# Kernel optimization log

Hardware: AMD Instinct MI355X
Metric: run time of the kernel (lower is better)

The kernel has to match this reference:

```python
import jax, jax.numpy as jnp
import numpy as np

NEG_INF = -9.0e15
ALPHA = 0.2  # leakyrelu slope


def setup_inputs() -> dict:
    key = jax.random.key(0)
    k1, k2, k3, k4, k5 = jax.random.split(key, 5)
    B, N, D_IN, D_OUT = 8, 2048, 128, 128
    h = jax.random.normal(k1, (B, N, D_IN), dtype=jnp.float32)
    adj = jax.random.randint(k2, (N, N), 0, 2, dtype=jnp.int32)
    W = jax.random.normal(k3, (D_IN, D_OUT), dtype=jnp.float32) * (1.0 / np.sqrt(D_IN))
    a_src = jax.random.normal(k4, (D_OUT,), dtype=jnp.float32) * (1.0 / np.sqrt(D_OUT))
    a_dst = jax.random.normal(k5, (D_OUT,), dtype=jnp.float32) * (1.0 / np.sqrt(D_OUT))
    return {"h": h, "adj": adj, "W": W, "a_src": a_src, "a_dst": a_dst}


def reference(h, adj, W, a_src, a_dst):
    # Wh: [B, N, D_out]
    Wh = jnp.einsum("bnd,de->bne", h, W)
    e_src = jnp.einsum("bne,e->bn", Wh, a_src)  # [B, N]
    e_dst = jnp.einsum("bne,e->bn", Wh, a_dst)  # [B, N]
    # additive attention logits: e[b,i,j] = e_src[b,i] + e_dst[b,j]
    e = e_src[:, :, None] + e_dst[:, None, :]  # [B, N, N]
    e = jnp.where(e > 0, e, ALPHA * e)  # leaky relu
    e = jnp.where(adj[None, :, :] > 0, e, NEG_INF)
    attention = jax.nn.softmax(e, axis=-1)  # [B, N, N]
    h_prime = jnp.einsum("bij,bje->bie", attention, Wh)
    return h_prime
```

## Files before the change

### kernel.cpp

```cpp
#include <hip/hip_runtime.h>
#include <stdint.h>

#define ALPHA 0.2f
#define LOG2E 1.4426950408889634f

typedef unsigned short u16;
typedef short s16x8 __attribute__((ext_vector_type(8)));
typedef float f32x4 __attribute__((ext_vector_type(4)));

union BF8 { s16x8 v; uint32_t u[4]; u16 s[8]; uint4 q; };

static __device__ __forceinline__ float bf2f(u16 u) {
  union { uint32_t i; float f; } c; c.i = ((uint32_t)u) << 16; return c.f;
}
static __device__ __forceinline__ uint32_t pk2bf(float lo, float hi) {
  uint32_t ul = __float_as_uint(lo) + 0x8000u;
  uint32_t uh = __float_as_uint(hi) + 0x8000u;
  return (ul >> 16) | (uh & 0xffff0000u);
}

static __device__ __forceinline__ void gl2lds16(const void* g, void* l) {
  __builtin_amdgcn_global_load_lds(
      (const __attribute__((address_space(1))) uint32_t*)g,
      (__attribute__((address_space(3))) uint32_t*)l, 16, 0, 0);
}

__global__ __launch_bounds__(256) void k_zero(uint32_t* __restrict__ out, int n32) {
  int gid = blockIdx.x * 256 + threadIdx.x;
  if (gid < n32) out[gid] = 0u;
}

__global__ __launch_bounds__(256) void k_prep(
    const int* __restrict__ adj, uint32_t* __restrict__ bits,
    const void* __restrict__ hV, const void* __restrict__ WgV,
    const void* __restrict__ aSrcV, const void* __restrict__ aDstV,
    int* __restrict__ flag,
    u16* __restrict__ WhT, float* __restrict__ eS, float* __restrict__ eD) {
  __shared__ __align__(16) char smemRaw[34816];
  __shared__ float aS[128], aD[128];

  const int tid = threadIdx.x;
  const int bk = blockIdx.x;

  if (bk >= 256) {
    const int pk = bk - 256;
    int base = pk * 256 + tid;
#pragma unroll
    for (int it = 0; it < 8; ++it) {
      int gid = base + it * (2048 * 256);
      unsigned long long m = __ballot(adj[gid] != 0);
      if ((tid & 63) == 0)
        *(unsigned long long*)(&bits[gid >> 5]) = m;
    }
    if (pk == 0 && tid < 64) {
      u16 v = ((const u16*)hV)[2 * tid];
      int e = (v >> 7) & 0xff;
      unsigned long long dm = __ballot(e >= 100 && e <= 140);
      if (tid == 0) flag[0] = (__popcll(dm) >= 48) ? 1 : 0;
    }
    return;
  }

  u16*   WT   = (u16*)smemRaw;
  float* tile = (float*)smemRaw;
  const int mb = bk * 64;

  int isBf;
  {
    u16 v = ((const u16*)hV)[2 * (tid & 63)];
    int e = (v >> 7) & 0xff;
    unsigned long long dm = __ballot(e >= 100 && e <= 140);
    isBf = (__popcll(dm) >= 48) ? 1 : 0;
  }

  if (isBf) {
    const u16* Wg = (const u16*)WgV;
    for (int it = 0; it < 8; ++it) {
      int idx = tid + it * 256;
      int k = idx >> 4, c0 = (idx & 15) * 8;
      uint4 w4 = *(const uint4*)(Wg + (k << 7) + c0);
      u16* wsv = (u16*)&w4;
#pragma unroll
      for (int e = 0; e < 8; ++e) WT[(c0 + e) * 136 + k] = wsv[e];
    }
    if (tid < 128) aS[tid] = bf2f(((const u16*)aSrcV)[tid]);
    else           aD[tid - 128] = bf2f(((const u16*)aDstV)[tid - 128]);
  } else {
    const float* Wg = (const float*)WgV;
    for (int it = 0; it < 8; ++it) {
      int idx = tid + it * 256;
      int k = idx >> 4, c0 = (idx & 15) * 8;
      float4 w0 = *(const float4*)(Wg + (k << 7) + c0);
      float4 w1 = *(const float4*)(Wg + (k << 7) + c0 + 4);
      float wf[8] = {w0.x, w0.y, w0.z, w0.w, w1.x, w1.y, w1.z, w1.w};
#pragma unroll
      for (int e = 0; e < 8; ++e)
        WT[(c0 + e) * 136 + k] = (u16)((__float_as_uint(wf[e]) + 0x8000u) >> 16);
    }
    if (tid < 128) aS[tid] = ((const float*)aSrcV)[tid];
    else           aD[tid - 128] = ((const float*)aDstV)[tid - 128];
  }
  __syncthreads();

  const int wv = tid >> 6, lane = tid & 63, ln = lane & 15, quad = lane >> 4;
  const int row = mb + wv * 16 + ln;

  f32x4 acc[8];
#pragma unroll
  for (int t = 0; t < 8; ++t) acc[t] = (f32x4){0.f, 0.f, 0.f, 0.f};

  if (isBf) {
    const u16* h = (const u16*)hV;
#pragma unroll
    for (int ks = 0; ks < 4; ++ks) {
      s16x8 af = *(const s16x8*)(h + (row << 7) + ks * 32 + quad * 8);
#pragma unroll
      for (int t = 0; t < 8; ++t) {
        s16x8 bfg = *(const s16x8*)(&WT[(t * 16 + ln) * 136 + ks * 32 + quad * 8]);
        acc[t] = __builtin_amdgcn_mfma_f32_16x16x32_bf16(af, bfg, acc[t], 0, 0, 0);
      }
    }
  } else {
    const float* h = (const float*)hV;
#pragma unroll
    for (int ks = 0; ks < 4; ++ks) {
      float4 a0 = *(const float4*)(h + (row << 7) + ks * 32 + quad * 8);
      float4 a1 = *(const float4*)(h + (row << 7) + ks * 32 + quad * 8 + 4);
      BF8 af;
      af.u[0] = pk2bf(a0.x, a0.y);
      af.u[1] = pk2bf(a0.z, a0.w);
      af.u[2] = pk2bf(a1.x, a1.y);
      af.u[3] = pk2bf(a1.z, a1.w);
#pragma unroll
      for (int t = 0; t < 8; ++t) {
        s16x8 bfg = *(const s16x8*)(&WT[(t * 16 + ln) * 136 + ks * 32 + quad * 8]);
        acc[t] = __builtin_amdgcn_mfma_f32_16x16x32_bf16(af.v, bfg, acc[t], 0, 0, 0);
      }
    }
  }
  __syncthreads();

#pragma unroll
  for (int t = 0; t < 8; ++t)
#pragma unroll
    for (int r = 0; r < 4; ++r)
      tile[(wv * 16 + quad * 4 + r) * 130 + t * 16 + ln] = acc[t][r];
  __syncthreads();

  if (tid < 128) {
    int r = tid & 63, grp = tid >> 6;
    const float* a = grp ? aD : aS;
    float sum = 0.f;
#pragma unroll 4
    for (int d = 0; d < 128; ++d) sum += tile[r * 130 + d] * a[d];
    int m = mb + r, b = m >> 11, n = m & 2047;
    (grp ? eD : eS)[(b << 11) + n] = sum * LOG2E;
  }

  {
    int d = tid >> 1, half = tid & 1;
    int n0 = mb & 2047, b = mb >> 11;
    uint32_t pk[16];
#pragma unroll
    for (int qq = 0; qq < 16; ++qq) {
      float v0 = tile[(half * 32 + 2 * qq) * 130 + d];
      float v1 = tile[(half * 32 + 2 * qq + 1) * 130 + d];
      pk[qq] = pk2bf(v0, v1);
    }
    uint4* dst = (uint4*)(WhT + (size_t)((b << 7) + d) * 2048 + n0 + half * 32);
#pragma unroll
    for (int c = 0; c < 4; ++c)
      dst[c] = make_uint4(pk[c * 4], pk[c * 4 + 1], pk[c * 4 + 2], pk[c * 4 + 3]);
  }
}

__global__ __launch_bounds__(512, 4) void k_attn(
    const u16* __restrict__ WhT, const float* __restrict__ eSrc,
    const float* __restrict__ eDst, const uint32_t* __restrict__ adjBits,
    const int* __restrict__ flag, void* __restrict__ outV) {
  __shared__ __align__(16) u16 bufB[2][8192];
  __shared__ __align__(16) u16 bufP[2][2048];

  const int tid = threadIdx.x;
  const int bid = (blockIdx.x & 7) * 64 + (blockIdx.x >> 3);
  const int b = bid >> 6, ig = bid & 63;
  const int i0 = ig * 32;

  const int w = tid >> 6, l = tid & 63;
  const int ln = l & 15, quad = l >> 4;
  const int s = w & 1, dh = w >> 1;

  const int gsrc = (l & 7) ^ ((l >> 3) & 7);
  const u16* whtB = WhT + ((size_t)b << 18);
  const u16* srcB = whtB + (size_t)(w * 8 + (l >> 3)) * 2048 + gsrc * 8;

  const int prow = tid >> 4, hg = tid & 15;
  const float sSp = eSrc[(b << 11) + i0 + prow];
  const float* eDb = eDst + (b << 11) + hg * 4;
  const uint32_t* adjB = adjBits + (size_t)(i0 + prow) * 64 + (hg >> 3);
  const int pOff = prow * 128 + ((hg ^ ((prow & 7) << 1)) * 8);

  const int aOff0 = (s * 16 + ln) * 128 + (((0 * 4 + quad) ^ (ln & 7)) * 16);
  const int aOff1 = (s * 16 + ln) * 128 + (((1 * 4 + quad) ^ (ln & 7)) * 16);
  const int bOff00 = (dh * 32 + 0 * 16 + ln) * 128 + (((0 * 4 + quad) ^ (ln & 7)) * 16);
  const int bOff10 = (dh * 32 + 1 * 16 + ln) * 128 + (((0 * 4 + quad) ^ (ln & 7)) * 16);
  const int bOff01 = (dh * 32 + 0 * 16 + ln) * 128 + (((1 * 4 + quad) ^ (ln & 7)) * 16);
  const int bOff11 = (dh * 32 + 1 * 16 + ln) * 128 + (((1 * 4 + quad) ^ (ln & 7)) * 16);

  f32x4 acc0 = (f32x4){0.f, 0.f, 0.f, 0.f};
  f32x4 acc1 = (f32x4){0.f, 0.f, 0.f, 0.f};
  f32x4 accD = (f32x4){0.f, 0.f, 0.f, 0.f};

  BF8 ones;
  ones.u[0] = 0x3f803f80u; ones.u[1] = 0x3f803f80u;
  ones.u[2] = 0x3f803f80u; ones.u[3] = 0x3f803f80u;

#define PPROD(dv, aw, pdst)  {                                                \
    uint32_t nib = ((aw) >> ((hg & 7) * 4)) & 0xfu;                           \
    float x0 = sSp + (dv)[0], x1 = sSp + (dv)[1];                             \
    float x2 = sSp + (dv)[2], x3 = sSp + (dv)[3];                             \
    float p0 = exp2f(__builtin_amdgcn_fmed3f(x0, ALPHA * x0, 80.f));          \
    float p1 = exp2f(__builtin_amdgcn_fmed3f(x1, ALPHA * x1, 80.f));          \
    float p2 = exp2f(__builtin_amdgcn_fmed3f(x2, ALPHA * x2, 80.f));          \
    float p3 = exp2f(__builtin_amdgcn_fmed3f(x3, ALPHA * x3, 80.f));          \
    uint32_t m01 = ((nib & 1u) ? 0x0000ffffu : 0u) | ((nib & 2u) ? 0xffff0000u : 0u); \
    uint32_t m23 = ((nib & 4u) ? 0x0000ffffu : 0u) | ((nib & 8u) ? 0xffff0000u : 0u); \
    *(uint2*)((char*)(pdst) + pOff) = make_uint2(pk2bf(p0, p1) & m01,         \
                                                 pk2bf(p2, p3) & m23);        \
  }

#define CONSUME(pPc, pBc)  {                                                  \
    s16x8 af0 = *(const s16x8*)((const char*)(pPc) + aOff0);                  \
    s16x8 af1 = *(const s16x8*)((const char*)(pPc) + aOff1);                  \
    s16x8 b00 = *(const s16x8*)((const char*)(pBc) + bOff00);                 \
    s16x8 b10 = *(const s16x8*)((const char*)(pBc) + bOff10);                 \
    s16x8 b01 = *(const s16x8*)((const char*)(pBc) + bOff01);                 \
    s16x8 b11 = *(const s16x8*)((const char*)(pBc) + bOff11);                 \
    __builtin_amdgcn_s_setprio(1);                                            \
    acc0 = __builtin_amdgcn_mfma_f32_16x16x32_bf16(af0, b00, acc0, 0, 0, 0);  \
    acc1 = __builtin_amdgcn_mfma_f32_16x16x32_bf16(af0, b10, acc1, 0, 0, 0);  \
    acc0 = __builtin_amdgcn_mfma_f32_16x16x32_bf16(af1, b01, acc0, 0, 0, 0);  \
    acc1 = __builtin_amdgcn_mfma_f32_16x16x32_bf16(af1, b11, acc1, 0, 0, 0);  \
    if (dh == 0) {                                                            \
      accD = __builtin_amdgcn_mfma_f32_16x16x32_bf16(af0, ones.v, accD, 0, 0, 0); \
      accD = __builtin_amdgcn_mfma_f32_16x16x32_bf16(af1, ones.v, accD, 0, 0, 0); \
    }                                                                         \
    __builtin_amdgcn_s_setprio(0);                                            \
  }

  u16 *bBc = bufB[0], *bBn = bufB[1];
  u16 *bPc = bufP[0], *bPn = bufP[1];

  gl2lds16(srcB, bBc + w * 512);
  gl2lds16(srcB + 131072, bBc + 4096 + w * 512);
  {
    f32x4 dv = *(const f32x4*)(eDb);
    uint32_t aw = adjB[0];
    PPROD(dv, aw, bPc);
  }
  __syncthreads();

  for (int t = 0; t < 32; ++t) {
    if (t + 1 < 32) {
      gl2lds16(srcB + (size_t)(t + 1) * 64, bBn + w * 512);
      gl2lds16(srcB + (size_t)(t + 1) * 64 + 131072, bBn + 4096 + w * 512);
      f32x4 dv = *(const f32x4*)(eDb + (t + 1) * 64);
      uint32_t aw = adjB[(t + 1) * 2];
      PPROD(dv, aw, bPn);
    }
    CONSUME(bPc, bBc);
    __syncthreads();
    u16* tb = bBc; bBc = bBn; bBn = tb;
    u16* tp = bPc; bPc = bPn; bPn = tp;
  }

  float* den = (float*)bufP;
  if (dh == 0 && ln == 0) {
#pragma unroll
    for (int r = 0; r < 4; ++r) den[s * 16 + quad * 4 + r] = accD[r];
  }
  __syncthreads();

  float inv[4];
#pragma unroll
  for (int r = 0; r < 4; ++r)
    inv[r] = 1.0f / fmaxf(den[s * 16 + quad * 4 + r], 1e-37f);

  const int isBf = *flag;
  if (isBf) {
    u16* outp = (u16*)outV;
#pragma unroll
    for (int tt = 0; tt < 2; ++tt) {
      f32x4 a = tt ? acc1 : acc0;
#pragma unroll
      for (int r = 0; r < 4; ++r) {
        size_t off = ((size_t)((b << 11) + i0 + s * 16 + quad * 4 + r) << 7)
                   + dh * 32 + tt * 16 + ln;
        float v = a[r] * inv[r];
        outp[off] = (u16)((__float_as_uint(v) + 0x8000u) >> 16);
      }
    }
  } else {
    float* outp = (float*)outV;
#pragma unroll
    for (int tt = 0; tt < 2; ++tt) {
      f32x4 a = tt ? acc1 : acc0;
#pragma unroll
      for (int r = 0; r < 4; ++r) {
        size_t off = ((size_t)((b << 11) + i0 + s * 16 + quad * 4 + r) << 7)
                   + dh * 32 + tt * 16 + ln;
        outp[off] = a[r] * inv[r];
      }
    }
  }
#undef PPROD
#undef CONSUME
}

extern "C" void kernel_launch(void* const* d_in, const int* in_sizes, int n_in,
                              void* d_out, int out_size, void* d_ws, size_t ws_size,
                              hipStream_t stream) {
  const void* h   = d_in[0];
  const int* adj  = (const int*)d_in[1];
  const void* Wg  = d_in[2];
  const void* aS  = d_in[3];
  const void* aD  = d_in[4];

  const size_t OFF_ES   = (size_t)4 << 20;
  const size_t OFF_ED   = OFF_ES + (64 << 10);
  const size_t OFF_BITS = OFF_ED + (64 << 10);
  const size_t OFF_FLAG = OFF_BITS + (512 << 10);
  const size_t NEEDED   = OFF_FLAG + 64;

  if (ws_size < NEEDED) {
    int n32 = out_size / 2;
    k_zero<<<(n32 + 255) / 256, 256, 0, stream>>>((uint32_t*)d_out, n32);
    return;
  }

  char* ws = (char*)d_ws;
  u16* WhT      = (u16*)ws;
  float* eSp    = (float*)(ws + OFF_ES);
  float* eDp    = (float*)(ws + OFF_ED);
  uint32_t* bit = (uint32_t*)(ws + OFF_BITS);
  int* flag     = (int*)(ws + OFF_FLAG);

  k_prep<<<2304, 256, 0, stream>>>(adj, bit, h, Wg, aS, aD, flag, WhT, eSp, eDp);
  k_attn<<<512, 512, 0, stream>>>(WhT, eSp, eDp, bit, flag, d_out);
}
```

Baseline: 116.2 us.

## Use 32x32x16 MFMA with split-K waves and compute softmax denominator on VALU

Replaces the 16x16x32 MFMA tiling (waves split by row half and column quarter, plus extra MFMAs against a ones vector for the denominator) with 32x32x16 MFMAs, where each wave covers all 32 rows for a 32-column slice and half of the K chunk. The two K-halves are reduced through shared memory at the end. The softmax denominator is now accumulated in scalar registers from the bf16-rounded probabilities and reduced with shuffles, which removes the extra denominator MFMAs. This cuts LDS fragment loads and MFMA count per step, in exchange for a final cross-wave merge and some added VALU work in the probability stage.

```diff
diff --git a/kernel.cpp b/kernel.cpp
--- a/kernel.cpp
+++ b/kernel.cpp
@@ -7,6 +7,7 @@
 typedef unsigned short u16;
 typedef short s16x8 __attribute__((ext_vector_type(8)));
 typedef float f32x4 __attribute__((ext_vector_type(4)));
+typedef float f32x16 __attribute__((ext_vector_type(16)));
 
 union BF8 { s16x8 v; uint32_t u[4]; u16 s[8]; uint4 q; };
 
@@ -180,6 +181,7 @@
     const int* __restrict__ flag, void* __restrict__ outV) {
   __shared__ __align__(16) u16 bufB[2][8192];
   __shared__ __align__(16) u16 bufP[2][2048];
+  __shared__ float den[32];
 
   const int tid = threadIdx.x;
   const int bid = (blockIdx.x & 7) * 64 + (blockIdx.x >> 3);
@@ -187,8 +189,9 @@
   const int i0 = ig * 32;
 
   const int w = tid >> 6, l = tid & 63;
-  const int ln = l & 15, quad = l >> 4;
-  const int s = w & 1, dh = w >> 1;
+  const int dh = w & 3, jh = w >> 2;
+  const int lh = l >> 5;
+  const int xk = l & 7;
 
   const int gsrc = (l & 7) ^ ((l >> 3) & 7);
   const u16* whtB = WhT + ((size_t)b << 18);
@@ -199,23 +202,18 @@
   const float* eDb = eDst + (b << 11) + hg * 4;
   const uint32_t* adjB = adjBits + (size_t)(i0 + prow) * 64 + (hg >> 3);
   const int pOff = prow * 128 + ((hg ^ ((prow & 7) << 1)) * 8);
-
-  const int aOff0 = (s * 16 + ln) * 128 + (((0 * 4 + quad) ^ (ln & 7)) * 16);
-  const int aOff1 = (s * 16 + ln) * 128 + (((1 * 4 + quad) ^ (ln & 7)) * 16);
-  const int bOff00 = (dh * 32 + 0 * 16 + ln) * 128 + (((0 * 4 + quad) ^ (ln & 7)) * 16);
-  const int bOff10 = (dh * 32 + 1 * 16 + ln) * 128 + (((0 * 4 + quad) ^ (ln & 7)) * 16);
-  const int bOff01 = (dh * 32 + 0 * 16 + ln) * 128 + (((1 * 4 + quad) ^ (ln & 7)) * 16);
-  const int bOff11 = (dh * 32 + 1 * 16 + ln) * 128 + (((1 * 4 + quad) ^ (ln & 7)) * 16);
-
-  f32x4 acc0 = (f32x4){0.f, 0.f, 0.f, 0.f};
-  f32x4 acc1 = (f32x4){0.f, 0.f, 0.f, 0.f};
-  f32x4 accD = (f32x4){0.f, 0.f, 0.f, 0.f};
-
-  BF8 ones;
-  ones.u[0] = 0x3f803f80u; ones.u[1] = 0x3f803f80u;
-  ones.u[2] = 0x3f803f80u; ones.u[3] = 0x3f803f80u;
-
-#define PPROD(dv, aw, pdst)  {                                                \
+  float dsum = 0.f;
+
+  const int aOff0 = (l & 31) * 128 + (((jh * 4 + 0 + lh) ^ xk) * 16);
+  const int aOff1 = (l & 31) * 128 + (((jh * 4 + 2 + lh) ^ xk) * 16);
+  const int bOff0 = (dh * 32 + (l & 31)) * 128 + (((jh * 4 + 0 + lh) ^ xk) * 16);
+  const int bOff1 = (dh * 32 + (l & 31)) * 128 + (((jh * 4 + 2 + lh) ^ xk) * 16);
+
+  f32x16 acc;
+#pragma unroll
+  for (int r = 0; r < 16; ++r) acc[r] = 0.f;
+
+#define PPROD(dv, aw, pdst) {                                                 \
     uint32_t nib = ((aw) >> ((hg & 7) * 4)) & 0xfu;                           \
     float x0 = sSp + (dv)[0], x1 = sSp + (dv)[1];                             \
     float x2 = sSp + (dv)[2], x3 = sSp + (dv)[3];                             \
@@ -223,29 +221,14 @@
     float p1 = exp2f(__builtin_amdgcn_fmed3f(x1, ALPHA * x1, 80.f));          \
     float p2 = exp2f(__builtin_amdgcn_fmed3f(x2, ALPHA * x2, 80.f));          \
     float p3 = exp2f(__builtin_amdgcn_fmed3f(x3, ALPHA * x3, 80.f));          \
-    uint32_t m01 = ((nib & 1u) ? 0x0000ffffu : 0u) | ((nib & 2u) ? 0xffff0000u : 0u); \
-    uint32_t m23 = ((nib & 4u) ? 0x0000ffffu : 0u) | ((nib & 8u) ? 0xffff0000u : 0u); \
-    *(uint2*)((char*)(pdst) + pOff) = make_uint2(pk2bf(p0, p1) & m01,         \
-                                                 pk2bf(p2, p3) & m23);        \
-  }
-
-#define CONSUME(pPc, pBc)  {                                                  \
-    s16x8 af0 = *(const s16x8*)((const char*)(pPc) + aOff0);                  \
-    s16x8 af1 = *(const s16x8*)((const char*)(pPc) + aOff1);                  \
-    s16x8 b00 = *(const s16x8*)((const char*)(pBc) + bOff00);                 \
-    s16x8 b10 = *(const s16x8*)((const char*)(pBc) + bOff10);                 \
-    s16x8 b01 = *(const s16x8*)((const char*)(pBc) + bOff01);                 \
-    s16x8 b11 = *(const s16x8*)((const char*)(pBc) + bOff11);                 \
-    __builtin_amdgcn_s_setprio(1);                                            \
-    acc0 = __builtin_amdgcn_mfma_f32_16x16x32_bf16(af0, b00, acc0, 0, 0, 0);  \
-    acc1 = __builtin_amdgcn_mfma_f32_16x16x32_bf16(af0, b10, acc1, 0, 0, 0);  \
-    acc0 = __builtin_amdgcn_mfma_f32_16x16x32_bf16(af1, b01, acc0, 0, 0, 0);  \
-    acc1 = __builtin_amdgcn_mfma_f32_16x16x32_bf16(af1, b11, acc1, 0, 0, 0);  \
-    if (dh == 0) {                                                            \
-      accD = __builtin_amdgcn_mfma_f32_16x16x32_bf16(af0, ones.v, accD, 0, 0, 0); \
-      accD = __builtin_amdgcn_mfma_f32_16x16x32_bf16(af1, ones.v, accD, 0, 0, 0); \
-    }                                                                         \
-    __builtin_amdgcn_s_setprio(0);                                            \
+    p0 = (nib & 1u) ? p0 : 0.f;                                               \
+    p1 = (nib & 2u) ? p1 : 0.f;                                               \
+    p2 = (nib & 4u) ? p2 : 0.f;                                               \
+    p3 = (nib & 8u) ? p3 : 0.f;                                               \
+    uint32_t w0 = pk2bf(p0, p1), w1 = pk2bf(p2, p3);                          \
+    dsum += __uint_as_float(w0 << 16) + __uint_as_float(w0 & 0xffff0000u)     \
+          + __uint_as_float(w1 << 16) + __uint_as_float(w1 & 0xffff0000u);    \
+    *(uint2*)((char*)(pdst) + pOff) = make_uint2(w0, w1);                     \
   }
 
   u16 *bBc = bufB[0], *bBn = bufB[1];
@@ -268,53 +251,59 @@
       uint32_t aw = adjB[(t + 1) * 2];
       PPROD(dv, aw, bPn);
     }
-    CONSUME(bPc, bBc);
+    {
+      s16x8 a0 = *(const s16x8*)((const char*)bPc + aOff0);
+      s16x8 a1 = *(const s16x8*)((const char*)bPc + aOff1);
+      s16x8 f0 = *(const s16x8*)((const char*)bBc + bOff0);
+      s16x8 f1 = *(const s16x8*)((const char*)bBc + bOff1);
+      __builtin_amdgcn_s_setprio(1);
+      acc = __builtin_amdgcn_mfma_f32_32x32x16_bf16(a0, f0, acc, 0, 0, 0);
+      acc = __builtin_amdgcn_mfma_f32_32x32x16_bf16(a1, f1, acc, 0, 0, 0);
+      __builtin_amdgcn_s_setprio(0);
+    }
     __syncthreads();
     u16* tb = bBc; bBc = bBn; bBn = tb;
     u16* tp = bPc; bPc = bPn; bPn = tp;
   }
 
-  float* den = (float*)bufP;
-  if (dh == 0 && ln == 0) {
-#pragma unroll
-    for (int r = 0; r < 4; ++r) den[s * 16 + quad * 4 + r] = accD[r];
-  }
-  __syncthreads();
-
-  float inv[4];
-#pragma unroll
-  for (int r = 0; r < 4; ++r)
-    inv[r] = 1.0f / fmaxf(den[s * 16 + quad * 4 + r], 1e-37f);
-
-  const int isBf = *flag;
-  if (isBf) {
-    u16* outp = (u16*)outV;
-#pragma unroll
-    for (int tt = 0; tt < 2; ++tt) {
-      f32x4 a = tt ? acc1 : acc0;
-#pragma unroll
-      for (int r = 0; r < 4; ++r) {
-        size_t off = ((size_t)((b << 11) + i0 + s * 16 + quad * 4 + r) << 7)
-                   + dh * 32 + tt * 16 + ln;
-        float v = a[r] * inv[r];
+  {
+#pragma unroll
+    for (int m = 1; m < 16; m <<= 1) dsum += __shfl_xor(dsum, m);
+    if ((tid & 15) == 0) den[prow] = dsum;
+  }
+  float* mrg = (float*)bufB;
+  if (jh == 1) {
+#pragma unroll
+    for (int r = 0; r < 16; ++r) mrg[dh * 1024 + r * 64 + l] = acc[r];
+  }
+  __syncthreads();
+
+  if (jh == 0) {
+    const int isBf = *flag;
+    const int col = dh * 32 + (l & 31);
+    if (isBf) {
+      u16* outp = (u16*)outV;
+#pragma unroll
+      for (int r = 0; r < 16; ++r) {
+        int irow = (r & 3) + 8 * (r >> 2) + 4 * lh;
+        float v = acc[r] + mrg[dh * 1024 + r * 64 + l];
+        v *= 1.0f / fmaxf(den[irow], 1e-37f);
+        size_t off = ((size_t)((b << 11) + i0 + irow) << 7) + col;
         outp[off] = (u16)((__float_as_uint(v) + 0x8000u) >> 16);
       }
-    }
-  } else {
-    float* outp = (float*)outV;
-#pragma unroll
-    for (int tt = 0; tt < 2; ++tt) {
-      f32x4 a = tt ? acc1 : acc0;
-#pragma unroll
-      for (int r = 0; r < 4; ++r) {
-        size_t off = ((size_t)((b << 11) + i0 + s * 16 + quad * 4 + r) << 7)
-                   + dh * 32 + tt * 16 + ln;
-        outp[off] = a[r] * inv[r];
+    } else {
+      float* outp = (float*)outV;
+#pragma unroll
+      for (int r = 0; r < 16; ++r) {
+        int irow = (r & 3) + 8 * (r >> 2) + 4 * lh;
+        float v = acc[r] + mrg[dh * 1024 + r * 64 + l];
+        v *= 1.0f / fmaxf(den[irow], 1e-37f);
+        size_t off = ((size_t)((b << 11) + i0 + irow) << 7) + col;
+        outp[off] = v;
       }
     }
   }
 #undef PPROD
-#undef CONSUME
 }
 
 extern "C" void kernel_launch(void* const* d_in, const int* in_sizes, int n_in,
```

After: 116.4 us. No clear change (+0.2%).
